# Optimization experiments

Measured on AMD Instinct MI355X. Metric: run time of the kernel, lower is better.

## Reference

```python
import jax, jax.numpy as jnp
import numpy as np

SR = 16000
BLOCK_SIZE = 160
N_WT = 64
WT_LEN = 512
SEC = 60
T = SR * SEC  # 960000 samples
FRAMES = 100 * SEC  # 6000 attention frames


def _make_sine_table(length, cycle, phase):
    i = np.arange(length, dtype=np.float32)
    wt = np.sin(cycle * 2 * np.pi * i / length + 2 * phase * np.pi).astype(np.float32)
    wt[-1] = wt[0]  # loop-closing trick: last sample = first sample
    return wt


def setup_inputs() -> dict:
    key = jax.random.key(0)
    k1, k2, k3, k4 = jax.random.split(key, 4)
    pitch = jax.random.uniform(k1, (1, T, 1), dtype=jnp.float32) * 360.0 + 40.0  # 40..400 Hz
    amplitude = jax.random.uniform(k2, (1, T, 1), dtype=jnp.float32)
    # wavetables: first 4 are fixed sine harmonics with wrapped endpoint, rest learned
    rng = np.random.default_rng(0)
    wts = np.asarray(jax.random.normal(k3, (N_WT, WT_LEN), dtype=jnp.float32)) * 0.01
    for idx in range(4):
        wts[idx] = _make_sine_table(WT_LEN, idx + 1, rng.uniform(0.0, 1.0))
    wts[4:, -1] = wts[4:, 0]  # wrap endpoint for learned tables too
    attention = jax.random.normal(k4, (N_WT, FRAMES), dtype=jnp.float32)
    return {
        "pitch": pitch,
        "amplitude": amplitude,
        "wavetables": jnp.asarray(wts),
        "attention": attention,
        "sec": SEC,
    }


def reference(pitch, amplitude, wavetables, attention, sec):
    L = wavetables.shape[1]
    freq = pitch.reshape(-1)  # [T], torch .squeeze()
    inc = freq / SR * L  # phase increment per sample
    # exclusive cumulative sum: cumsum(inc) - inc  (matches cumsum - increment[0] broadcast)
    idx = (jnp.cumsum(inc) - inc) % L  # [T]
    lo = jnp.floor(idx)
    hi = jnp.ceil(idx)
    alpha = idx - lo  # fractional part
    lo_i = lo.astype(jnp.int32)
    hi_i = hi.astype(jnp.int32) % L
    # tanh applied to learned tables (idx >= 4); fixed sine tables passed through
    wts_eff = jnp.concatenate([wavetables[:4], jnp.tanh(wavetables[4:])], axis=0)  # [64, L]
    w_lo = wts_eff[:, lo_i]  # [64, T] gather
    w_hi = wts_eff[:, hi_i]  # [64, T] gather
    osc = w_lo + alpha[None, :] * (w_hi - w_lo)  # [64, T] linear interp
    att = jax.nn.softmax(attention, axis=0)  # softmax over wavetables
    att_up = jnp.repeat(att, BLOCK_SIZE, axis=1)  # nearest-neighbor upsample -> [64, T]
    mixed = jnp.sum(osc * att_up, axis=0)  # [T]
    return mixed[None, :, None] * amplitude  # [1, T, 1]
```

## Files before the change

kernel.cpp:

```cpp
#include <hip/hip_runtime.h>
#include <math.h>

#define BLKSZ 160
#define NWT   64
#define WTLEN 512
#define FPB   24
#define SPB   3840
#define NTHR  768
#define SMP   28

#define NB1   3750
#define NB1P  3760
#define NB2   235
#define NB2P  240
#define NB3   15

static __device__ __forceinline__ float inc32_of(float p) {
    return (p / 16000.0f) * 512.0f;
}

__global__ __launch_bounds__(256) void k_leaf(
    const float* __restrict__ pitch, const float* __restrict__ wts,
    float* __restrict__ bs1, float* __restrict__ wts_eff, int T)
{
    int t = threadIdx.x;
    if (blockIdx.x >= NB2) {
        int i = (blockIdx.x - NB2) * 256 + t;
        if (i < NWT * WTLEN) {
            float v = wts[i];
            if ((i >> 9) >= 4) v = tanhf(v);
            wts_eff[i] = v;
        }
        return;
    }
    __shared__ float b0[256];
    int blk = blockIdx.x;
    size_t s0 = (size_t)blk * 4096;
    int nsamp = min(4096, T - (int)s0);
    int nb0 = nsamp >> 4;
    if (t < nb0) {
        const float4* p4 = (const float4*)(pitch + s0 + (size_t)t * 16);
        float acc = 0.f;
        #pragma unroll
        for (int i = 0; i < 4; ++i) {
            float4 v = p4[i];
            acc = acc + inc32_of(v.x);
            acc = acc + inc32_of(v.y);
            acc = acc + inc32_of(v.z);
            acc = acc + inc32_of(v.w);
        }
        b0[t] = acc;
    }
    __syncthreads();
    int nb1 = nb0 >> 4;
    if (t < nb1) {
        float acc = b0[t * 16];
        for (int j = 1; j < 16; ++j) acc = acc + b0[t * 16 + j];
        bs1[blk * 16 + t] = acc;
    }
}

__global__ __launch_bounds__(768, 3) void k_main(
    const float* __restrict__ pitch, const float* __restrict__ amp,
    const float* __restrict__ att, const float* __restrict__ wts_eff,
    const float* __restrict__ bs1g, float* __restrict__ out, int frames)
{
    __shared__ float smT[NWT][SMP];
    __shared__ float mixrow[FPB][WTLEN];
    __shared__ float pr[SPB];
    __shared__ float roffL[SPB / 16];
    __shared__ float bs2L[NB2P];
    __shared__ float bs3L[NB3];
    __shared__ float S4L[NB3];
    __shared__ float S3w[2];
    __shared__ float S2w[16];
    __shared__ float bs1prevL;

    float* bs1L = &mixrow[0][0];

    int tid = threadIdx.x, lane = tid & 63, wv = tid >> 6;
    int b = blockIdx.x;
    int f0 = b * FPB;
    size_t base = (size_t)b * SPB;
    int j0 = 15 * b - 2;
    int rlo = max(j0, 0) >> 4;

    #pragma unroll
    for (int r = 0; r < 2; ++r) {
        int f = f0 + wv * 2 + r;
        float a = att[(size_t)lane * frames + f];
        float m = a;
        #pragma unroll
        for (int off = 32; off; off >>= 1) m = fmaxf(m, __shfl_xor(m, off, 64));
        float e = expf(a - m);
        float s = e;
        #pragma unroll
        for (int off = 32; off; off >>= 1) s += __shfl_xor(s, off, 64);
        smT[lane][wv * 2 + r] = e / s;
    }

    float increg[SPB / NTHR];
    #pragma unroll
    for (int i = 0; i < SPB / NTHR; ++i) {
        increg[i] = inc32_of(pitch[base + i * NTHR + tid]);
        pr[i * NTHR + tid] = increg[i];
    }
    for (int i = tid; i < NB1P; i += NTHR)
        bs1L[i] = (i < NB1) ? bs1g[i] : 0.f;
    __syncthreads();

    if (tid < SPB / 16) {
        int bofs = tid * 16;
        float acc = pr[bofs];
        for (int j = 1; j < 16; ++j) { acc = acc + pr[bofs + j]; pr[bofs + j] = acc; }
    }
    if (tid >= 272 && tid < 272 + NB2P) {
        int t2 = tid - 272;
        float a = 0.f;
        if (t2 < NB2) {
            a = bs1L[t2 * 16];
            for (int j = 1; j < 16; ++j) a = a + bs1L[t2 * 16 + j];
        }
        bs2L[t2] = a;
    }
    __syncthreads();
    if (tid < NB3) {
        float a = bs2L[tid * 16];
        for (int j = 1; j < 16; ++j) a = a + bs2L[tid * 16 + j];
        bs3L[tid] = a;
    }
    __syncthreads();
    if (tid == 0) {
        float a = 0.f;
        for (int i = 0; i < NB3; ++i) { a = a + bs3L[i]; S4L[i] = a; }
    }
    __syncthreads();
    if (tid < 2) {
        int r = rlo - 1 + tid;
        float v = 0.f;
        if (r >= 0 && r < NB2) {
            int g = r >> 4, p = r & 15;
            float a = bs2L[g * 16];
            for (int k = 1; k <= p; ++k) a = a + bs2L[g * 16 + k];
            v = g ? (a + S4L[g - 1]) : a;
        }
        S3w[tid] = v;
    }
    if (tid == 2) bs1prevL = (b > 0) ? bs1L[15 * b - 1] : 0.f;
    __syncthreads();
    if (tid < 16) {
        int j = j0 + tid;
        float v = 0.f;
        if (j >= 0) {
            int r = j >> 4, p = j & 15;
            float a = bs1L[r * 16];
            for (int q = 1; q <= p; ++q) a = a + bs1L[r * 16 + q];
            v = r ? (a + S3w[r - rlo]) : a;
        }
        S2w[tid] = v;
    }
    __syncthreads();

    if (tid < SPB / 16) {
        float v;
        if (tid == 0) {
            v = (b == 0) ? 0.f : (bs1prevL + S2w[0]);
        } else {
            int lr = (tid - 1) >> 4;
            int p  = (tid - 1) & 15;
            float acc = pr[(lr * 16) * 16 + 15];
            for (int q = 1; q <= p; ++q) acc = acc + pr[(lr * 16 + q) * 16 + 15];
            int gr = 15 * b + lr;
            v = gr ? (acc + S2w[lr + 1]) : acc;
        }
        roffL[tid] = v;
    }
    {
        #pragma unroll
        for (int it = 0; it < 2; ++it) {
            int item = tid + it * NTHR;
            int fg = item >> 9;
            int j  = item & 511;
            float acc[8];
            #pragma unroll
            for (int k = 0; k < 8; ++k) acc[k] = 0.f;
            for (int w = 0; w < NWT; ++w) {
                float v = wts_eff[w * WTLEN + j];
                float4 s0 = *(const float4*)&smT[w][fg * 8];
                float4 s1 = *(const float4*)&smT[w][fg * 8 + 4];
                acc[0] += s0.x * v;  acc[1] += s0.y * v;
                acc[2] += s0.z * v;  acc[3] += s0.w * v;
                acc[4] += s1.x * v;  acc[5] += s1.y * v;
                acc[6] += s1.z * v;  acc[7] += s1.w * v;
            }
            #pragma unroll
            for (int k = 0; k < 8; ++k) mixrow[fg * 8 + k][j] = acc[k];
        }
    }
    __syncthreads();

    #pragma unroll
    for (int i = 0; i < SPB / NTHR; ++i) {
        int tl = i * NTHR + tid;
        size_t tg = base + tl;
        float C = pr[tl] + roffL[tl >> 4];
        float sub = C - increg[i];
        float idx = fmodf(sub, 512.0f);
        if (idx < 0.f) idx += 512.f;
        int li = (int)idx;
        float alpha = idx - (float)li;
        int hi = ((int)ceilf(idx)) & (WTLEN - 1);
        int fr = tl / BLKSZ;
        float wlo = mixrow[fr][li];
        float whi = mixrow[fr][hi];
        out[tg] = (wlo + alpha * (whi - wlo)) * amp[tg];
    }
}

extern "C" void kernel_launch(void* const* d_in, const int* in_sizes, int n_in,
                              void* d_out, int out_size, void* d_ws, size_t ws_size,
                              hipStream_t stream) {
    const float* pitch = (const float*)d_in[0];
    const float* amp   = (const float*)d_in[1];
    const float* wts   = (const float*)d_in[2];
    const float* att   = (const float*)d_in[3];

    int T      = in_sizes[0];
    int frames = T / BLKSZ;
    int nmain  = T / SPB;

    float* ws      = (float*)d_ws;
    float* wts_eff = ws;
    float* bs1     = ws + 32768;
    float* out     = (float*)d_out;

    int nwts_blocks = (NWT * WTLEN + 255) / 256;
    k_leaf<<<NB2 + nwts_blocks, 256, 0, stream>>>(pitch, wts, bs1, wts_eff, T);
    k_main<<<nmain, 768, 0, stream>>>(pitch, amp, att, wts_eff, bs1, out, frames);
}
```

Baseline: 25.57 us.

## Fuse pitch block-sum pass into main kernel via grid-wide atomic barrier

Drops the separate leaf kernel that reduced pitch increments into 16x16 block sums. Each main block now computes its own 15 block sums from the shared-memory prefix, writes them to global memory and waits at a spin-wait atomic grid barrier before reading every block's sums. This avoids reading pitch twice and removes one kernel's worth of work. In exchange it depends on all 250 blocks being resident at once, since otherwise the barrier deadlocks, and it adds spin-wait latency.

```diff
diff --git a/kernel.cpp b/kernel.cpp
--- a/kernel.cpp
+++ b/kernel.cpp
@@ -7,6 +7,7 @@
 #define FPB   24
 #define SPB   3840
 #define NTHR  768
+#define NBLK  250
 #define SMP   28
 
 #define NB1   3750
@@ -19,51 +20,25 @@
     return (p / 16000.0f) * 512.0f;
 }
 
-__global__ __launch_bounds__(256) void k_leaf(
-    const float* __restrict__ pitch, const float* __restrict__ wts,
-    float* __restrict__ bs1, float* __restrict__ wts_eff, int T)
+__global__ __launch_bounds__(256) void k_prep(
+    const float* __restrict__ wts, float* __restrict__ wts_eff,
+    unsigned int* __restrict__ counter)
 {
-    int t = threadIdx.x;
-    if (blockIdx.x >= NB2) {
-        int i = (blockIdx.x - NB2) * 256 + t;
-        if (i < NWT * WTLEN) {
-            float v = wts[i];
-            if ((i >> 9) >= 4) v = tanhf(v);
-            wts_eff[i] = v;
-        }
+    if (blockIdx.x == 128) {
+        if (threadIdx.x == 0) counter[0] = 0u;
         return;
     }
-    __shared__ float b0[256];
-    int blk = blockIdx.x;
-    size_t s0 = (size_t)blk * 4096;
-    int nsamp = min(4096, T - (int)s0);
-    int nb0 = nsamp >> 4;
-    if (t < nb0) {
-        const float4* p4 = (const float4*)(pitch + s0 + (size_t)t * 16);
-        float acc = 0.f;
-        #pragma unroll
-        for (int i = 0; i < 4; ++i) {
-            float4 v = p4[i];
-            acc = acc + inc32_of(v.x);
-            acc = acc + inc32_of(v.y);
-            acc = acc + inc32_of(v.z);
-            acc = acc + inc32_of(v.w);
-        }
-        b0[t] = acc;
-    }
-    __syncthreads();
-    int nb1 = nb0 >> 4;
-    if (t < nb1) {
-        float acc = b0[t * 16];
-        for (int j = 1; j < 16; ++j) acc = acc + b0[t * 16 + j];
-        bs1[blk * 16 + t] = acc;
-    }
-}
-
-__global__ __launch_bounds__(768, 3) void k_main(
+    int i = blockIdx.x * 256 + threadIdx.x;
+    float v = wts[i];
+    if ((i >> 9) >= 4) v = tanhf(v);
+    wts_eff[i] = v;
+}
+
+__global__ __launch_bounds__(768, 3) void k_fused(
     const float* __restrict__ pitch, const float* __restrict__ amp,
     const float* __restrict__ att, const float* __restrict__ wts_eff,
-    const float* __restrict__ bs1g, float* __restrict__ out, int frames)
+    float* __restrict__ bs1g, unsigned int* __restrict__ counter,
+    float* __restrict__ out, int frames)
 {
     __shared__ float smT[NWT][SMP];
     __shared__ float mixrow[FPB][WTLEN];
@@ -105,8 +80,6 @@
         increg[i] = inc32_of(pitch[base + i * NTHR + tid]);
         pr[i * NTHR + tid] = increg[i];
     }
-    for (int i = tid; i < NB1P; i += NTHR)
-        bs1L[i] = (i < NB1) ? bs1g[i] : 0.f;
     __syncthreads();
 
     if (tid < SPB / 16) {
@@ -114,14 +87,42 @@
         float acc = pr[bofs];
         for (int j = 1; j < 16; ++j) { acc = acc + pr[bofs + j]; pr[bofs + j] = acc; }
     }
-    if (tid >= 272 && tid < 272 + NB2P) {
-        int t2 = tid - 272;
+    __syncthreads();
+
+    if (tid < 15) {
+        float acc = pr[(tid * 16) * 16 + 15];
+        for (int q = 1; q < 16; ++q) acc = acc + pr[(tid * 16 + q) * 16 + 15];
+        bs1g[15 * b + tid] = acc;
+    }
+    __syncthreads();
+
+    if (tid == 0) {
+        __threadfence();
+        __hip_atomic_fetch_add(&counter[0], 1u, __ATOMIC_RELEASE,
+                               __HIP_MEMORY_SCOPE_AGENT);
+        while (__hip_atomic_load(&counter[0], __ATOMIC_ACQUIRE,
+                                 __HIP_MEMORY_SCOPE_AGENT) < (unsigned)NBLK) {
+            __builtin_amdgcn_s_sleep(8);
+        }
+    }
+    __syncthreads();
+
+    for (int i = tid; i < NB1P; i += NTHR) {
+        float v = 0.f;
+        if (i < NB1)
+            v = __hip_atomic_load(&bs1g[i], __ATOMIC_RELAXED,
+                                  __HIP_MEMORY_SCOPE_AGENT);
+        bs1L[i] = v;
+    }
+    __syncthreads();
+
+    if (tid < NB2P) {
         float a = 0.f;
-        if (t2 < NB2) {
-            a = bs1L[t2 * 16];
-            for (int j = 1; j < 16; ++j) a = a + bs1L[t2 * 16 + j];
-        }
-        bs2L[t2] = a;
+        if (tid < NB2) {
+            a = bs1L[tid * 16];
+            for (int j = 1; j < 16; ++j) a = a + bs1L[tid * 16 + j];
+        }
+        bs2L[tid] = a;
     }
     __syncthreads();
     if (tid < NB3) {
@@ -227,14 +228,14 @@
 
     int T      = in_sizes[0];
     int frames = T / BLKSZ;
-    int nmain  = T / SPB;
 
     float* ws      = (float*)d_ws;
     float* wts_eff = ws;
     float* bs1     = ws + 32768;
+    unsigned int* counter = (unsigned int*)(ws + 32768 + 3840);
     float* out     = (float*)d_out;
 
-    int nwts_blocks = (NWT * WTLEN + 255) / 256;
-    k_leaf<<<NB2 + nwts_blocks, 256, 0, stream>>>(pitch, wts, bs1, wts_eff, T);
-    k_main<<<nmain, 768, 0, stream>>>(pitch, amp, att, wts_eff, bs1, out, frames);
-}
+    k_prep <<<129, 256, 0, stream>>>(wts, wts_eff, counter);
+    k_fused<<<NBLK, NTHR, 0, stream>>>(pitch, amp, att, wts_eff, bs1, counter,
+                                       out, frames);
+}
```

Measured after the change: 41.59 us. 1.63x slower.

## Shrink main-kernel tiles to 8 frames per block and pad scan arrays

Applied to the files above, without the earlier changes.

Each main-kernel block now handles 8 attention frames (1280 samples) with 256 threads instead of 24 frames with 768 threads. This triples the grid so work spreads over more CUs. Shared prefix-scan arrays get one padding slot per 16 entries to avoid bank conflicts in the strided per-thread scans. The cost is that every block still loads the full level-1 block-sum array and recomputes the upper scan levels, so that redundant work is repeated three times as often.

```diff
diff --git a/kernel.cpp b/kernel.cpp
--- a/kernel.cpp
+++ b/kernel.cpp
@@ -4,16 +4,18 @@
 #define BLKSZ 160
 #define NWT   64
 #define WTLEN 512
-#define FPB   24
-#define SPB   3840
-#define NTHR  768
-#define SMP   28
+#define FPB   8
+#define SPB   1280
+#define NTHR  256
+#define SMP   12
 
 #define NB1   3750
 #define NB1P  3760
 #define NB2   235
 #define NB2P  240
 #define NB3   15
+
+#define PRI(a)  ((a) + ((a) >> 4))
 
 static __device__ __forceinline__ float inc32_of(float p) {
     return (p / 16000.0f) * 512.0f;
@@ -60,20 +62,20 @@
     }
 }
 
-__global__ __launch_bounds__(768, 3) void k_main(
+__global__ __launch_bounds__(256) void k_main(
     const float* __restrict__ pitch, const float* __restrict__ amp,
     const float* __restrict__ att, const float* __restrict__ wts_eff,
     const float* __restrict__ bs1g, float* __restrict__ out, int frames)
 {
     __shared__ float smT[NWT][SMP];
     __shared__ float mixrow[FPB][WTLEN];
-    __shared__ float pr[SPB];
+    __shared__ float pr[SPB + SPB / 16];
     __shared__ float roffL[SPB / 16];
     __shared__ float bs2L[NB2P];
     __shared__ float bs3L[NB3];
     __shared__ float S4L[NB3];
     __shared__ float S3w[2];
-    __shared__ float S2w[16];
+    __shared__ float S2w[6];
     __shared__ float bs1prevL;
 
     float* bs1L = &mixrow[0][0];
@@ -82,7 +84,7 @@
     int b = blockIdx.x;
     int f0 = b * FPB;
     size_t base = (size_t)b * SPB;
-    int j0 = 15 * b - 2;
+    int j0 = 5 * b - 2;
     int rlo = max(j0, 0) >> 4;
 
     #pragma unroll
@@ -103,25 +105,31 @@
     #pragma unroll
     for (int i = 0; i < SPB / NTHR; ++i) {
         increg[i] = inc32_of(pitch[base + i * NTHR + tid]);
-        pr[i * NTHR + tid] = increg[i];
+        pr[PRI(i * NTHR + tid)] = increg[i];
     }
     for (int i = tid; i < NB1P; i += NTHR)
-        bs1L[i] = (i < NB1) ? bs1g[i] : 0.f;
+        bs1L[PRI(i)] = (i < NB1) ? bs1g[i] : 0.f;
     __syncthreads();
 
     if (tid < SPB / 16) {
-        int bofs = tid * 16;
-        float acc = pr[bofs];
-        for (int j = 1; j < 16; ++j) { acc = acc + pr[bofs + j]; pr[bofs + j] = acc; }
-    }
-    if (tid >= 272 && tid < 272 + NB2P) {
-        int t2 = tid - 272;
-        float a = 0.f;
-        if (t2 < NB2) {
-            a = bs1L[t2 * 16];
-            for (int j = 1; j < 16; ++j) a = a + bs1L[t2 * 16 + j];
-        }
-        bs2L[t2] = a;
+        int a0 = tid * 17;
+        float acc = pr[a0];
+        for (int j = 1; j < 16; ++j) { acc = acc + pr[a0 + j]; pr[a0 + j] = acc; }
+    } else {
+        #pragma unroll
+        for (int rep = 0; rep < 2; ++rep) {
+            int c = (tid - 80) + rep * 176;
+            if (rep == 1 && c >= NB2P) break;
+            if (c < NB2P) {
+                float a = 0.f;
+                if (c < NB2) {
+                    int a0 = c * 17;
+                    a = bs1L[a0];
+                    for (int j = 1; j < 16; ++j) a = a + bs1L[a0 + j];
+                }
+                bs2L[c] = a;
+            }
+        }
     }
     __syncthreads();
     if (tid < NB3) {
@@ -146,15 +154,16 @@
         }
         S3w[tid] = v;
     }
-    if (tid == 2) bs1prevL = (b > 0) ? bs1L[15 * b - 1] : 0.f;
-    __syncthreads();
-    if (tid < 16) {
+    if (tid == 2) bs1prevL = (b > 0) ? bs1L[PRI(5 * b - 1)] : 0.f;
+    __syncthreads();
+    if (tid < 6) {
         int j = j0 + tid;
         float v = 0.f;
         if (j >= 0) {
             int r = j >> 4, p = j & 15;
-            float a = bs1L[r * 16];
-            for (int q = 1; q <= p; ++q) a = a + bs1L[r * 16 + q];
+            int a0 = r * 17;
+            float a = bs1L[a0];
+            for (int q = 1; q <= p; ++q) a = a + bs1L[a0 + q];
             v = r ? (a + S3w[r - rlo]) : a;
         }
         S2w[tid] = v;
@@ -168,9 +177,9 @@
         } else {
             int lr = (tid - 1) >> 4;
             int p  = (tid - 1) & 15;
-            float acc = pr[(lr * 16) * 16 + 15];
-            for (int q = 1; q <= p; ++q) acc = acc + pr[(lr * 16 + q) * 16 + 15];
-            int gr = 15 * b + lr;
+            float acc = pr[(lr * 16) * 17 + 15];
+            for (int q = 1; q <= p; ++q) acc = acc + pr[(lr * 16 + q) * 17 + 15];
+            int gr = 5 * b + lr;
             v = gr ? (acc + S2w[lr + 1]) : acc;
         }
         roffL[tid] = v;
@@ -178,23 +187,21 @@
     {
         #pragma unroll
         for (int it = 0; it < 2; ++it) {
-            int item = tid + it * NTHR;
-            int fg = item >> 9;
-            int j  = item & 511;
-            float acc[8];
+            int j = tid + it * NTHR;
+            float acc[FPB];
             #pragma unroll
-            for (int k = 0; k < 8; ++k) acc[k] = 0.f;
+            for (int k = 0; k < FPB; ++k) acc[k] = 0.f;
             for (int w = 0; w < NWT; ++w) {
                 float v = wts_eff[w * WTLEN + j];
-                float4 s0 = *(const float4*)&smT[w][fg * 8];
-                float4 s1 = *(const float4*)&smT[w][fg * 8 + 4];
+                float4 s0 = *(const float4*)&smT[w][0];
+                float4 s1 = *(const float4*)&smT[w][4];
                 acc[0] += s0.x * v;  acc[1] += s0.y * v;
                 acc[2] += s0.z * v;  acc[3] += s0.w * v;
                 acc[4] += s1.x * v;  acc[5] += s1.y * v;
                 acc[6] += s1.z * v;  acc[7] += s1.w * v;
             }
             #pragma unroll
-            for (int k = 0; k < 8; ++k) mixrow[fg * 8 + k][j] = acc[k];
+            for (int k = 0; k < FPB; ++k) mixrow[k][j] = acc[k];
         }
     }
     __syncthreads();
@@ -203,7 +210,7 @@
     for (int i = 0; i < SPB / NTHR; ++i) {
         int tl = i * NTHR + tid;
         size_t tg = base + tl;
-        float C = pr[tl] + roffL[tl >> 4];
+        float C = pr[PRI(tl)] + roffL[tl >> 4];
         float sub = C - increg[i];
         float idx = fmodf(sub, 512.0f);
         if (idx < 0.f) idx += 512.f;
@@ -236,5 +243,5 @@
 
     int nwts_blocks = (NWT * WTLEN + 255) / 256;
     k_leaf<<<NB2 + nwts_blocks, 256, 0, stream>>>(pitch, wts, bs1, wts_eff, T);
-    k_main<<<nmain, 768, 0, stream>>>(pitch, amp, att, wts_eff, bs1, out, frames);
-}
+    k_main<<<nmain, 256, 0, stream>>>(pitch, amp, att, wts_eff, bs1, out, frames);
+}
```

Result: slower. 29.09 us (+13.8%).
